# Kernel tuning notes

Hardware: AMD Instinct MI355X
Metric: run time of the kernel (lower is better)

The kernel has to match this reference:

```python
import jax, jax.numpy as jnp
import numpy as np

EPS = 1e-12   # F.normalize default eps
TH = 0.5      # forward-arg default threshold
CLAMP_LO, CLAMP_HI = 0.01, 0.999


def setup_inputs() -> dict:
    key = jax.random.key(0)
    k1, k2 = jax.random.split(key)
    # x4: ResNet layer3 features after ala1 scaling + upfeat, stride-16 of a 1024px image
    x4 = jax.random.normal(k1, (8, 1024, 64, 64), dtype=jnp.float32)
    # logits: classifier output after upfeat, same spatial grid, 21 classes
    logits = jax.random.normal(k2, (8, 21, 64, 64), dtype=jnp.float32)
    return {"x4": x4, "logits": logits, "pcm": 2}


def reference(x4, logits, pcm):
    b, c, h, w = x4.shape
    hw = h * w
    xf = x4.reshape(b, c, hw)                      # [b, c, hw]
    # F.normalize(dim=1): x / max(||x||_2, eps)
    norm = jnp.sqrt(jnp.sum(xf * xf, axis=1, keepdims=True))
    xn = xf / jnp.maximum(norm, EPS)
    # pixel affinity: [b, hw, hw]
    aff = jnp.einsum('bci,bcj->bij', xn, xn)
    aff = jnp.clip(aff, CLAMP_LO, CLAMP_HI)
    aff = jnp.where(aff < TH, jnp.zeros((), aff.dtype), aff)
    # column-normalize (torch sum over dim=1)
    aff = aff / jnp.sum(aff, axis=1, keepdims=True)
    lf = logits.reshape(b, -1, hw)                 # [b, K, hw]
    for _ in range(pcm):                           # pcm is a Python int
        lf = jnp.einsum('bki,bij->bkj', lf, aff)
    return lf.reshape(b, -1, h, w)
```

## Files before the change

### kernel.cpp

```cpp
#include <hip/hip_runtime.h>
#include <hip/hip_bf16.h>

#define B_   8
#define C_   1024
#define HW_  4096
#define NK   21
#define NT   32
#define NTRI (NT * (NT + 1) / 2)

using bf16 = __hip_bfloat16;
typedef __attribute__((ext_vector_type(4))) float float4_;
typedef __attribute__((ext_vector_type(8))) int int8v;

#define WAITV0() asm volatile("s_waitcnt vmcnt(0)" ::: "memory")
#define FENCE()  asm volatile("" ::: "memory")
#define BARRIER() do { FENCE(); __builtin_amdgcn_s_barrier(); FENCE(); } while (0)

__global__ __launch_bounds__(256) void ktrans(const float* __restrict__ x4, float* __restrict__ sumsq,
                                              unsigned char* __restrict__ Xq) {
    int b = blockIdx.z, ct = blockIdx.y, jt = blockIdx.x;
    int c0 = ct * 128, j0 = jt * 64;
    int t = threadIdx.x;
    __shared__ float tile[128][65];
    __shared__ float ssq[64];

    int jl = t & 63, cl = t >> 6;
    if (t < 64) ssq[t] = 0.f;
    __syncthreads();
    float part = 0.f;
#pragma unroll
    for (int cc = 0; cc < 128; cc += 4) {
        float v = x4[((size_t)b * C_ + c0 + cc + cl) * HW_ + j0 + jl];
        tile[cc + cl][jl] = v;
        part = fmaf(v, v, part);
    }
    atomicAdd(&ssq[jl], part);
    __syncthreads();

    int j = t >> 2, q = t & 3;
    int jg = j0 + j;
    unsigned int pk[8];
#pragma unroll
    for (int g = 0; g < 8; ++g) {
        float f0 = tile[q * 32 + g * 4 + 0][j];
        float f1 = tile[q * 32 + g * 4 + 1][j];
        float f2 = tile[q * 32 + g * 4 + 2][j];
        float f3 = tile[q * 32 + g * 4 + 3][j];
        unsigned int r = 0;
        r = __builtin_amdgcn_cvt_pk_fp8_f32(f0, f1, r, false);
        r = __builtin_amdgcn_cvt_pk_fp8_f32(f2, f3, r, true);
        pk[g] = r;
    }
    unsigned char* dst = Xq + ((size_t)b * HW_ + jg) * C_ + c0 + q * 32;
    *(uint4*)(dst)      = make_uint4(pk[0], pk[1], pk[2], pk[3]);
    *(uint4*)(dst + 16) = make_uint4(pk[4], pk[5], pk[6], pk[7]);

    if (t < 64) atomicAdd(&sumsq[b * HW_ + j0 + t], ssq[t]);
}

__global__ __launch_bounds__(256, 2) void kgram(const unsigned char* __restrict__ Xq,
                                                const float* __restrict__ sumsq, bf16* __restrict__ aff,
                                                float* __restrict__ colsum, int* __restrict__ flags) {
    int lin = blockIdx.x;
    int b = lin & 7;
    int p = lin >> 3;
    int it = (int)((2.0f * NT + 1.0f - sqrtf((2.0f * NT + 1.0f) * (2.0f * NT + 1.0f) - 8.0f * (float)p)) * 0.5f);
    while (it > 0 && p < it * NT - it * (it - 1) / 2) --it;
    while (p >= (it + 1) * NT - (it + 1) * it / 2) ++it;
    int jt = it + p - (it * NT - it * (it - 1) / 2);

    int i0 = it * 128, j0 = jt * 128;
    int tid = threadIdx.x, w = tid >> 6, l = tid & 63;
    int wr = w >> 1, wc = w & 1;
    int lrow = l & 15, lk = l >> 4;

    __shared__ __align__(16) unsigned char smem[2][32768];
    __shared__ int fl;

    const unsigned char* XA = Xq + ((size_t)b * HW_ + i0) * C_;
    const unsigned char* XB = Xq + ((size_t)b * HW_ + j0) * C_;

    int rhi = tid >> 3, sl = tid & 7;

    auto stg = [&](unsigned char* buf, int k0) {
#pragma unroll
        for (int q = 0; q < 4; ++q) {
            int R = q * 32 + rhi;
            int gp = sl ^ (R & 7);
            __builtin_amdgcn_global_load_lds(
                (const __attribute__((address_space(1))) void*)(XA + (size_t)R * C_ + k0 + (gp << 4)),
                (__attribute__((address_space(3))) void*)(buf + R * 128 + (sl << 4)), 16, 0, 0);
            __builtin_amdgcn_global_load_lds(
                (const __attribute__((address_space(1))) void*)(XB + (size_t)R * C_ + k0 + (gp << 4)),
                (__attribute__((address_space(3))) void*)(buf + 16384 + R * 128 + (sl << 4)), 16, 0, 0);
        }
    };

    auto ldfrag = [&](const unsigned char* base, int r) {
        int sw = r & 7;
        uint4 lo = *(const uint4*)(base + r * 128 + (((lk * 2) ^ sw) << 4));
        uint4 hi = *(const uint4*)(base + r * 128 + (((lk * 2 + 1) ^ sw) << 4));
        int8v v; v[0] = lo.x; v[1] = lo.y; v[2] = lo.z; v[3] = lo.w;
        v[4] = hi.x; v[5] = hi.y; v[6] = hi.z; v[7] = hi.w;
        return v;
    };

    float4_ acc[4][4];
#pragma unroll
    for (int m = 0; m < 4; ++m)
#pragma unroll
        for (int n = 0; n < 4; ++n) acc[m][n] = {0.f, 0.f, 0.f, 0.f};

    stg(smem[0], 0);
    WAITV0();
    BARRIER();

    for (int kt = 0; kt < 8; ++kt) {
        unsigned char* cur = smem[kt & 1];
        if (kt < 7) stg(smem[(kt + 1) & 1], (kt + 1) * 128);

        int8v bv[4];
#pragma unroll
        for (int n = 0; n < 4; ++n) bv[n] = ldfrag(cur + 16384, wc * 64 + n * 16 + lrow);
        __builtin_amdgcn_s_setprio(1);
#pragma unroll
        for (int m = 0; m < 4; ++m) {
            int8v av = ldfrag(cur, wr * 64 + m * 16 + lrow);
#pragma unroll
            for (int n = 0; n < 4; ++n)
                acc[m][n] = __builtin_amdgcn_mfma_scale_f32_16x16x128_f8f6f4(
                    av, bv[n], acc[m][n], 0, 0, 0, 0x7f7f7f7f, 0, 0x7f7f7f7f);
        }
        __builtin_amdgcn_s_setprio(0);

        if (kt < 7) WAITV0();
        BARRIER();
    }

    float rnj[4];
#pragma unroll
    for (int n = 0; n < 4; ++n) {
        int j = j0 + wc * 64 + n * 16 + lrow;
        rnj[n] = 1.0f / fmaxf(sqrtf(sumsq[b * HW_ + j]), 1e-12f);
    }
    float rni[4][4];
#pragma unroll
    for (int m = 0; m < 4; ++m)
#pragma unroll
        for (int r = 0; r < 4; ++r) {
            int i = i0 + wr * 64 + m * 16 + lk * 4 + r;
            rni[m][r] = 1.0f / fmaxf(sqrtf(sumsq[b * HW_ + i]), 1e-12f);
        }
    bool any = false;
#pragma unroll
    for (int m = 0; m < 4; ++m)
#pragma unroll
        for (int n = 0; n < 4; ++n)
#pragma unroll
            for (int r = 0; r < 4; ++r) {
                acc[m][n][r] *= rni[m][r] * rnj[n];
                any |= (acc[m][n][r] >= 0.5f);
            }

    if (tid == 0) fl = 0;
    __syncthreads();
    unsigned long long bal = __ballot(any);
    if (l == 0 && bal != 0ull) atomicOr(&fl, 1);
    __syncthreads();
    bool mirror = (it != jt);
    if (tid == 0) {
        flags[(b * NT + it) * NT + jt] = fl;
        if (mirror) flags[(b * NT + jt) * NT + it] = fl;
    }

    if (fl) {
        size_t affb = (size_t)b * HW_ * HW_;
        float rsum[4][4];
#pragma unroll
        for (int m = 0; m < 4; ++m)
#pragma unroll
            for (int r = 0; r < 4; ++r) rsum[m][r] = 0.f;

#pragma unroll
        for (int n = 0; n < 4; ++n) {
            int j = j0 + wc * 64 + n * 16 + lrow;
            float cs = 0.f;
#pragma unroll
            for (int m = 0; m < 4; ++m) {
#pragma unroll
                for (int r = 0; r < 4; ++r) {
                    float v = acc[m][n][r];
                    v = fminf(fmaxf(v, 0.01f), 0.999f);
                    v = (v < 0.5f) ? 0.0f : v;
                    bf16 bb = __float2bfloat16(v);
                    unsigned short us = __builtin_bit_cast(unsigned short, bb);
                    int i = i0 + wr * 64 + m * 16 + lk * 4 + r;
                    __builtin_nontemporal_store(us, (unsigned short*)(aff + affb + (size_t)i * HW_ + j));
                    float bf = __bfloat162float(bb);
                    cs += bf;
                    rsum[m][r] += bf;
                    if (mirror)
                        __builtin_nontemporal_store(us, (unsigned short*)(aff + affb + (size_t)j * HW_ + i));
                }
            }
            cs += __shfl_xor(cs, 16);
            cs += __shfl_xor(cs, 32);
            if (lk == 0) atomicAdd(&colsum[b * HW_ + j], cs);
        }
        if (mirror) {
#pragma unroll
            for (int m = 0; m < 4; ++m) {
#pragma unroll
                for (int r = 0; r < 4; ++r) {
                    float s = rsum[m][r];
                    s += __shfl_xor(s, 1);
                    s += __shfl_xor(s, 2);
                    s += __shfl_xor(s, 4);
                    s += __shfl_xor(s, 8);
                    if (lrow == 0) {
                        int i = i0 + wr * 64 + m * 16 + lk * 4 + r;
                        atomicAdd(&colsum[b * HW_ + i], s);
                    }
                }
            }
        }
    }
}

__global__ __launch_bounds__(128) void kprop(const float* __restrict__ lf, const bf16* __restrict__ aff,
                                             const int* __restrict__ flags, const float* __restrict__ colsum,
                                             float* __restrict__ outp) {
    int b = blockIdx.y, jt = blockIdx.x;
    int t = threadIdx.x;
    int j = jt * 128 + t;
    __shared__ float lfs[NK * 128];
    float acc[NK];
#pragma unroll
    for (int k = 0; k < NK; ++k) acc[k] = 0.f;

    for (int it = 0; it < NT; ++it) {
        if (flags[(b * NT + it) * NT + jt] == 0) continue;
        __syncthreads();
        for (int idx = t; idx < NK * 128; idx += 128)
            lfs[idx] = lf[((size_t)b * NK + (idx >> 7)) * HW_ + it * 128 + (idx & 127)];
        __syncthreads();
        const bf16* ap = aff + ((size_t)b * HW_ + it * 128) * HW_ + j;
        for (int ii = 0; ii < 128; ++ii) {
            float a = __bfloat162float(ap[(size_t)ii * HW_]);
#pragma unroll
            for (int k = 0; k < NK; ++k)
                acc[k] = fmaf(lfs[(k << 7) + ii], a, acc[k]);
        }
    }
    float inv = 1.0f / colsum[b * HW_ + j];
#pragma unroll
    for (int k = 0; k < NK; ++k)
        outp[((size_t)b * NK + k) * HW_ + j] = acc[k] * inv;
}

extern "C" void kernel_launch(void* const* d_in, const int* in_sizes, int n_in,
                              void* d_out, int out_size, void* d_ws, size_t ws_size,
                              hipStream_t stream) {
    const float* x4 = (const float*)d_in[0];
    const float* logits = (const float*)d_in[1];
    float* out = (float*)d_out;

    char* w = (char*)d_ws;
    size_t off = 0;
    auto take = [&](size_t bytes) {
        char* p = w + off;
        off += (bytes + 255) & ~(size_t)255;
        return p;
    };
    unsigned char* Xq = (unsigned char*)take((size_t)B_ * HW_ * C_);
    bf16* aff     = (bf16*)take((size_t)B_ * HW_ * HW_ * 2);
    float* colsum = (float*)take((size_t)B_ * HW_ * 4);
    int*   flags  = (int*)take((size_t)B_ * NT * NT * 4);
    float* sumsq  = (float*)take((size_t)B_ * HW_ * 4);
    float* lf1    = (float*)take((size_t)B_ * NK * HW_ * 4);

    hipMemsetAsync(colsum, 0,
                   (size_t)B_ * HW_ * 4 + (size_t)B_ * NT * NT * 4 + (size_t)B_ * HW_ * 4, stream);

    ktrans<<<dim3(HW_ / 64, C_ / 128, B_), dim3(256), 0, stream>>>(x4, sumsq, Xq);
    kgram <<<dim3(NTRI * B_), dim3(256), 0, stream>>>(Xq, sumsq, aff, colsum, flags);

    kprop<<<dim3(NT, B_), dim3(128), 0, stream>>>(logits, aff, flags, colsum, lf1);
    kprop<<<dim3(NT, B_), dim3(128), 0, stream>>>(lf1, aff, flags, colsum, out);
}
```

Before: 357.8 us.

## Restructure transpose, use cached aff stores, split prop reduction across waves

ktrans now has each block walk the full channel range for 32-pixel groups. It stages the fp8 output in shared memory and writes coalesced full rows, storing sumsq directly instead of through atomics, which removes that memset. kgram's affinity stores become normal cached stores instead of nontemporal ones, so the propagation kernels may hit in cache. kprop uses 256 threads over 64 columns, with four waves each covering a quarter of the row tile and a shared-memory reduction at the end. This doubles the grid from 256 to 512 blocks for better occupancy, at the cost of extra shared memory and a final sync.

```diff
diff --git a/kernel.cpp b/kernel.cpp
--- a/kernel.cpp
+++ b/kernel.cpp
@@ -18,44 +18,57 @@
 
 __global__ __launch_bounds__(256) void ktrans(const float* __restrict__ x4, float* __restrict__ sumsq,
                                               unsigned char* __restrict__ Xq) {
-    int b = blockIdx.z, ct = blockIdx.y, jt = blockIdx.x;
-    int c0 = ct * 128, j0 = jt * 64;
+    int jt = blockIdx.x, b = blockIdx.y;
+    int j0 = jt * 64;
     int t = threadIdx.x;
-    __shared__ float tile[128][65];
-    __shared__ float ssq[64];
-
-    int jl = t & 63, cl = t >> 6;
-    if (t < 64) ssq[t] = 0.f;
-    __syncthreads();
-    float part = 0.f;
-#pragma unroll
-    for (int cc = 0; cc < 128; cc += 4) {
-        float v = x4[((size_t)b * C_ + c0 + cc + cl) * HW_ + j0 + jl];
-        tile[cc + cl][jl] = v;
-        part = fmaf(v, v, part);
-    }
-    atomicAdd(&ssq[jl], part);
-    __syncthreads();
-
-    int j = t >> 2, q = t & 3;
-    int jg = j0 + j;
-    unsigned int pk[8];
-#pragma unroll
-    for (int g = 0; g < 8; ++g) {
-        float f0 = tile[q * 32 + g * 4 + 0][j];
-        float f1 = tile[q * 32 + g * 4 + 1][j];
-        float f2 = tile[q * 32 + g * 4 + 2][j];
-        float f3 = tile[q * 32 + g * 4 + 3][j];
-        unsigned int r = 0;
-        r = __builtin_amdgcn_cvt_pk_fp8_f32(f0, f1, r, false);
-        r = __builtin_amdgcn_cvt_pk_fp8_f32(f2, f3, r, true);
-        pk[g] = r;
-    }
-    unsigned char* dst = Xq + ((size_t)b * HW_ + jg) * C_ + c0 + q * 32;
-    *(uint4*)(dst)      = make_uint4(pk[0], pk[1], pk[2], pk[3]);
-    *(uint4*)(dst + 16) = make_uint4(pk[4], pk[5], pk[6], pk[7]);
-
-    if (t < 64) atomicAdd(&sumsq[b * HW_ + j0 + t], ssq[t]);
+    __shared__ float tin[128][33];
+    __shared__ unsigned int outw[32][260];
+    __shared__ float ssq[32];
+
+    int jl = t & 31, cl = t >> 5;
+    int qq = t >> 5, jq = t & 31;
+
+    for (int jg = 0; jg < 2; ++jg) {
+        int jbase = j0 + jg * 32;
+        if (t < 32) ssq[t] = 0.f;
+        float part = 0.f;
+
+        for (int ct = 0; ct < 8; ++ct) {
+            __syncthreads();
+#pragma unroll
+            for (int cc = 0; cc < 16; ++cc) {
+                float v = x4[((size_t)b * C_ + ct * 128 + cc * 8 + cl) * HW_ + jbase + jl];
+                tin[cc * 8 + cl][jl] = v;
+                part = fmaf(v, v, part);
+            }
+            __syncthreads();
+            unsigned int wv[4];
+#pragma unroll
+            for (int g = 0; g < 4; ++g) {
+                float f0 = tin[qq * 16 + g * 4 + 0][jq];
+                float f1 = tin[qq * 16 + g * 4 + 1][jq];
+                float f2 = tin[qq * 16 + g * 4 + 2][jq];
+                float f3 = tin[qq * 16 + g * 4 + 3][jq];
+                unsigned int r = 0;
+                r = __builtin_amdgcn_cvt_pk_fp8_f32(f0, f1, r, false);
+                r = __builtin_amdgcn_cvt_pk_fp8_f32(f2, f3, r, true);
+                wv[g] = r;
+            }
+            *(uint4*)&outw[jq][ct * 32 + qq * 4] = make_uint4(wv[0], wv[1], wv[2], wv[3]);
+        }
+        atomicAdd(&ssq[jl], part);
+        __syncthreads();
+
+#pragma unroll
+        for (int ps = 0; ps < 8; ++ps) {
+            int r = ps * 4 + (t >> 6);
+            int ch = t & 63;
+            uint4 v = *(const uint4*)&outw[r][ch * 4];
+            *(uint4*)(Xq + ((size_t)b * HW_ + jbase + r) * C_ + ch * 16) = v;
+        }
+        if (t < 32) sumsq[b * HW_ + jbase + t] = ssq[t];
+        __syncthreads();
+    }
 }
 
 __global__ __launch_bounds__(256, 2) void kgram(const unsigned char* __restrict__ Xq,
@@ -193,14 +206,12 @@
                     v = fminf(fmaxf(v, 0.01f), 0.999f);
                     v = (v < 0.5f) ? 0.0f : v;
                     bf16 bb = __float2bfloat16(v);
-                    unsigned short us = __builtin_bit_cast(unsigned short, bb);
                     int i = i0 + wr * 64 + m * 16 + lk * 4 + r;
-                    __builtin_nontemporal_store(us, (unsigned short*)(aff + affb + (size_t)i * HW_ + j));
+                    aff[affb + (size_t)i * HW_ + j] = bb;
                     float bf = __bfloat162float(bb);
                     cs += bf;
                     rsum[m][r] += bf;
-                    if (mirror)
-                        __builtin_nontemporal_store(us, (unsigned short*)(aff + affb + (size_t)j * HW_ + i));
+                    if (mirror) aff[affb + (size_t)j * HW_ + i] = bb;
                 }
             }
             cs += __shfl_xor(cs, 16);
@@ -227,35 +238,54 @@
     }
 }
 
-__global__ __launch_bounds__(128) void kprop(const float* __restrict__ lf, const bf16* __restrict__ aff,
+__global__ __launch_bounds__(256) void kprop(const float* __restrict__ lf, const bf16* __restrict__ aff,
                                              const int* __restrict__ flags, const float* __restrict__ colsum,
                                              float* __restrict__ outp) {
-    int b = blockIdx.y, jt = blockIdx.x;
+    int jt = blockIdx.x, b = blockIdx.y;
     int t = threadIdx.x;
-    int j = jt * 128 + t;
+    int q = t >> 6, jl = t & 63;
+    int j = jt * 64 + jl;
     __shared__ float lfs[NK * 128];
+    __shared__ float ps[3][NK][64];
     float acc[NK];
 #pragma unroll
     for (int k = 0; k < NK; ++k) acc[k] = 0.f;
 
     for (int it = 0; it < NT; ++it) {
-        if (flags[(b * NT + it) * NT + jt] == 0) continue;
+        if (flags[(b * NT + it) * NT + (jt >> 1)] == 0) continue;
         __syncthreads();
-        for (int idx = t; idx < NK * 128; idx += 128)
+        for (int idx = t; idx < NK * 128; idx += 256)
             lfs[idx] = lf[((size_t)b * NK + (idx >> 7)) * HW_ + it * 128 + (idx & 127)];
         __syncthreads();
-        const bf16* ap = aff + ((size_t)b * HW_ + it * 128) * HW_ + j;
-        for (int ii = 0; ii < 128; ++ii) {
-            float a = __bfloat162float(ap[(size_t)ii * HW_]);
+        const bf16* ap = aff + ((size_t)b * HW_ + it * 128 + q * 32) * HW_ + j;
+        for (int ii = 0; ii < 32; ii += 4) {
+            float a0 = __bfloat162float(ap[(size_t)(ii + 0) * HW_]);
+            float a1 = __bfloat162float(ap[(size_t)(ii + 1) * HW_]);
+            float a2 = __bfloat162float(ap[(size_t)(ii + 2) * HW_]);
+            float a3 = __bfloat162float(ap[(size_t)(ii + 3) * HW_]);
+            int base = (q * 32 + ii);
 #pragma unroll
             for (int k = 0; k < NK; ++k)
-                acc[k] = fmaf(lfs[(k << 7) + ii], a, acc[k]);
-        }
-    }
-    float inv = 1.0f / colsum[b * HW_ + j];
-#pragma unroll
-    for (int k = 0; k < NK; ++k)
-        outp[((size_t)b * NK + k) * HW_ + j] = acc[k] * inv;
+                acc[k] = fmaf(lfs[(k << 7) + base + 0], a0,
+                          fmaf(lfs[(k << 7) + base + 1], a1,
+                          fmaf(lfs[(k << 7) + base + 2], a2,
+                          fmaf(lfs[(k << 7) + base + 3], a3, acc[k]))));
+        }
+    }
+
+    if (q) {
+#pragma unroll
+        for (int k = 0; k < NK; ++k) ps[q - 1][k][jl] = acc[k];
+    }
+    __syncthreads();
+    if (q == 0) {
+        float inv = 1.0f / colsum[b * HW_ + j];
+#pragma unroll
+        for (int k = 0; k < NK; ++k) {
+            float s = acc[k] + ps[0][k][jl] + ps[1][k][jl] + ps[2][k][jl];
+            outp[((size_t)b * NK + k) * HW_ + j] = s * inv;
+        }
+    }
 }
 
 extern "C" void kernel_launch(void* const* d_in, const int* in_sizes, int n_in,
@@ -280,11 +310,11 @@
     float* lf1    = (float*)take((size_t)B_ * NK * HW_ * 4);
 
     hipMemsetAsync(colsum, 0,
-                   (size_t)B_ * HW_ * 4 + (size_t)B_ * NT * NT * 4 + (size_t)B_ * HW_ * 4, stream);
-
-    ktrans<<<dim3(HW_ / 64, C_ / 128, B_), dim3(256), 0, stream>>>(x4, sumsq, Xq);
+                   (size_t)B_ * HW_ * 4 + (size_t)B_ * NT * NT * 4, stream);
+
+    ktrans<<<dim3(64, B_), dim3(256), 0, stream>>>(x4, sumsq, Xq);
     kgram <<<dim3(NTRI * B_), dim3(256), 0, stream>>>(Xq, sumsq, aff, colsum, flags);
 
-    kprop<<<dim3(NT, B_), dim3(128), 0, stream>>>(logits, aff, flags, colsum, lf1);
-    kprop<<<dim3(NT, B_), dim3(128), 0, stream>>>(lf1, aff, flags, colsum, out);
+    kprop<<<dim3(64, B_), dim3(256), 0, stream>>>(logits, aff, flags, colsum, lf1);
+    kprop<<<dim3(64, B_), dim3(256), 0, stream>>>(lf1, aff, flags, colsum, out);
 }
```

After: 338.1 us. -5.5%, faster.
